# Performance work log

Measured on AMD Instinct MI355X. Metric: run time of the kernel, lower is better.

## Reference

```python
import jax, jax.numpy as jnp
import numpy as np

P = 8.0  # Lp exponent of the distance neuron (finite-p stage of l_inf-dist training)


def _patches(t, k, stride, pad):
    # [B, Cin, H, W] -> [B, Cin*k*k, H', W'], feature dim ordered channel-major
    return jax.lax.conv_general_dilated_patches(
        t, (k, k), (stride, stride), [(pad, pad), (pad, pad)])


def _lp(d):
    # d: [B, Cout, Cin*k*k, H', W'] nonnegative -> Lp norm over patch dim
    return jnp.power(jnp.sum(jnp.power(d, P), axis=2), 1.0 / P)


def norm_dist_conv(x, l, u, w, stride, pad):
    # Lp-distance "convolution": y[b,o,i,j] = || patch(x)[b,:,i,j] - w[o,:] ||_p
    # mean_normalize=True: zero-center each output unit's weight vector
    Cout, Cin, k, _ = w.shape
    wf = w.reshape(Cout, -1)
    wf = wf - jnp.mean(wf, axis=1, keepdims=True)
    wb = wf[None, :, :, None, None]                      # [1, Cout, Ckk, 1, 1]
    px = _patches(x, k, stride, pad)[:, None]            # [B, 1, Ckk, H', W']
    pl = _patches(l, k, stride, pad)[:, None]
    pu = _patches(u, k, stride, pad)[:, None]
    y = _lp(jnp.abs(px - wb))
    # interval bounds of |x_j - w_j| given x_j in [l_j, u_j], then monotone Lp
    dl = jnp.maximum(jnp.maximum(pl - wb, wb - pu), 0.0)
    du = jnp.maximum(jnp.abs(pl - wb), jnp.abs(pu - wb))
    return y, _lp(dl), _lp(du)


def bound_relu(x, l, u):
    # ReLU is monotone: apply elementwise to value and both bounds
    return jax.nn.relu(x), jax.nn.relu(l), jax.nn.relu(u)


def setup_inputs() -> dict:
    key = jax.random.key(0)
    k1, k2, k3 = jax.random.split(key, 3)
    B, C, H, W = 4, 32, 32, 32
    eps = 0.1  # l_inf perturbation radius
    x = jax.random.normal(k1, (B, C, H, W), dtype=jnp.float32)
    lower = x - eps
    upper = x + eps
    scale = 1.0 / np.sqrt(C * 9)
    weight1 = jax.random.normal(k2, (C, C, 3, 3), dtype=jnp.float32) * scale
    weight2 = jax.random.normal(k3, (C, C, 3, 3), dtype=jnp.float32) * scale
    return {"x": x, "lower": lower, "upper": upper,
            "weight1": weight1, "weight2": weight2}


def reference(x, lower, upper, weight1, weight2):
    # conv1 (stride=1, pad=1) -> BoundReLU -> conv2 -> residual add -> BoundReLU
    o = norm_dist_conv(x, lower, upper, weight1, 1, 1)
    o = bound_relu(*o)
    o = norm_dist_conv(*o, weight2, 1, 1)
    out = (o[0] + x, o[1] + lower, o[2] + upper)  # identity shortcut (stride=1, in==out)
    out = bound_relu(*out)
    return jnp.stack(out)  # [3, B, C, H, W]: (value, lower, upper)
```

## Files before the change

kernel.cpp:

```cpp
#include <hip/hip_runtime.h>
#include <hip/hip_bf16.h>

#define NB 4
#define NC 32
#define NH 32
#define NW 32
#define KK 288
#define PLANE (NB*NC*NH*NW)

__global__ __launch_bounds__(256) void prep_weights_k(
        const float* __restrict__ w1,
        const float* __restrict__ w2,
        float* __restrict__ wf1, float* __restrict__ wf2)
{
    const int row = blockIdx.x;
    const float* src = (row < NC) ? w1 : w2;
    float* dst = (row < NC) ? wf1 : wf2;
    const int co = row & (NC - 1);
    const int tid = threadIdx.x;
    __shared__ float red[256];
    const float a = (tid < KK)       ? src[co*KK + tid]       : 0.0f;
    const float b = (tid + 256 < KK) ? src[co*KK + tid + 256] : 0.0f;
    red[tid] = a + b;
    __syncthreads();
    for (int s = 128; s > 0; s >>= 1) {
        if (tid < s) red[tid] += red[tid + s];
        __syncthreads();
    }
    const float mean = red[0] * (1.0f / (float)KK);
    if (tid < KK)       dst[co*KK + tid]       = a - mean;
    if (tid + 256 < KK) dst[co*KK + tid + 256] = b - mean;
}

template<bool STAGE2>
__global__ __launch_bounds__(256) void normdist_conv_k(
    const float* __restrict__ xb,
    const float* __restrict__ lb,
    const float* __restrict__ ub,
    const float* __restrict__ my,
    const float* __restrict__ ml,
    const float* __restrict__ mu,
    const float* __restrict__ wf,
    float* __restrict__ oy, float* __restrict__ ol, float* __restrict__ ou,
    float* __restrict__ out)
{
    const int h   = blockIdx.x;
    const int cog = blockIdx.y;
    const int b   = blockIdx.z;
    const int tx  = threadIdx.x;
    const int ty  = threadIdx.y;
    const int tid = ty * 32 + tx;

    __shared__ float sX[NC*3*34];
    __shared__ float sL[NC*3*34];
    __shared__ float sU[NC*3*34];
    __shared__ float sW[8*KK];

    for (int i = tid; i < 8*KK; i += 256) sW[i] = wf[cog*8*KK + i];

    for (int i = tid; i < NC*3*34; i += 256) {
        const int c   = i / 102;
        const int rem = i - c*102;
        const int r   = rem / 34;
        const int col = rem - r*34;
        const int gh  = h + r - 1;
        const int gw  = col - 1;
        float vx = 0.0f, vl = 0.0f, vu = 0.0f;
        if ((unsigned)gh < NH && (unsigned)gw < NW) {
            const int g = ((b*NC + c)*NH + gh)*NW + gw;
            if (STAGE2) { vx = my[g]; vl = ml[g]; vu = mu[g]; }
            else        { vx = xb[g]; vl = lb[g]; vu = ub[g]; }
        }
        sX[i] = vx; sL[i] = vl; sU[i] = vu;
    }
    __syncthreads();

    float accY = 0.0f, accL = 0.0f, accU = 0.0f;
    const float* wrow = &sW[ty*KK];
    #pragma unroll 2
    for (int c = 0; c < NC; ++c) {
        #pragma unroll
        for (int r = 0; r < 3; ++r) {
            const int pb = (c*3 + r)*34 + tx;
            const int wb = c*9 + r*3;
            #pragma unroll
            for (int kw = 0; kw < 3; ++kw) {
                const float wv = wrow[wb + kw];
                const float px = sX[pb + kw];
                const float pl = sL[pb + kw];
                const float pu = sU[pb + kw];
                const float d  = px - wv;
                const float d2 = d*d, d4 = d2*d2;
                accY = fmaf(d4, d4, accY);
                const float a  = pl - wv;
                const float nb = wv - pu;
                const float m  = fmaxf(fmaxf(a, nb), 0.0f);
                const float m2 = m*m, m4 = m2*m2;
                accL = fmaf(m4, m4, accL);
                const float a2 = a*a, q2 = nb*nb;
                const float mm2 = fmaxf(a2, q2);
                const float mm4 = mm2*mm2;
                accU = fmaf(mm4, mm4, accU);
            }
        }
    }

    const float y  = sqrtf(sqrtf(sqrtf(accY)));
    const float dl = sqrtf(sqrtf(sqrtf(accL)));
    const float du = sqrtf(sqrtf(sqrtf(accU)));

    const int co = cog*8 + ty;
    const int o  = ((b*NC + co)*NH + h)*NW + tx;
    if (!STAGE2) {
        oy[o] = y; ol[o] = dl; ou[o] = du;
    } else {
        out[o]           = fmaxf(y  + xb[o], 0.0f);
        out[PLANE + o]   = fmaxf(dl + lb[o], 0.0f);
        out[2*PLANE + o] = fmaxf(du + ub[o], 0.0f);
    }
}

extern "C" void kernel_launch(void* const* d_in, const int* in_sizes, int n_in,
                              void* d_out, int out_size, void* d_ws, size_t ws_size,
                              hipStream_t stream)
{
    const float* x  = (const float*)d_in[0];
    const float* l  = (const float*)d_in[1];
    const float* u  = (const float*)d_in[2];
    const float* w1 = (const float*)d_in[3];
    const float* w2 = (const float*)d_in[4];
    float* ws  = (float*)d_ws;
    float* wf1 = ws;
    float* wf2 = ws + NC*KK;
    float* my  = ws + 2*NC*KK;
    float* ml  = my + PLANE;
    float* mu  = ml + PLANE;
    float* out = (float*)d_out;

    prep_weights_k<<<64, 256, 0, stream>>>(w1, w2, wf1, wf2);

    dim3 blk(32, 8);
    dim3 grd(NH, 4, NB);
    normdist_conv_k<false><<<grd, blk, 0, stream>>>(x, l, u, nullptr, nullptr, nullptr,
                                                    wf1, my, ml, mu, nullptr);
    normdist_conv_k<true ><<<grd, blk, 0, stream>>>(x, l, u, my, ml, mu,
                                                    wf2, nullptr, nullptr, nullptr, out);
}
```

Before: 109.9 us.

## Fuse weight mean-centering into conv kernels and pack x/l/u into float4 LDS

Removes the separate weight-preparation kernel launch: each conv block now loads raw weights and zero-centers them in shared memory with a warp-shuffle reduction. The x/lower/upper tiles are interleaved into one float4 shared array, and weights are padded to float4 per row, so the inner loop issues wide LDS loads instead of three scalar loads per tap. This trades one fewer launch and fewer LDS instructions for redundant mean computation in every block and a larger shared-memory footprint.

```diff
diff --git a/kernel.cpp b/kernel.cpp
--- a/kernel.cpp
+++ b/kernel.cpp
@@ -8,30 +8,6 @@
 #define KK 288
 #define PLANE (NB*NC*NH*NW)
 
-__global__ __launch_bounds__(256) void prep_weights_k(
-        const float* __restrict__ w1,
-        const float* __restrict__ w2,
-        float* __restrict__ wf1, float* __restrict__ wf2)
-{
-    const int row = blockIdx.x;
-    const float* src = (row < NC) ? w1 : w2;
-    float* dst = (row < NC) ? wf1 : wf2;
-    const int co = row & (NC - 1);
-    const int tid = threadIdx.x;
-    __shared__ float red[256];
-    const float a = (tid < KK)       ? src[co*KK + tid]       : 0.0f;
-    const float b = (tid + 256 < KK) ? src[co*KK + tid + 256] : 0.0f;
-    red[tid] = a + b;
-    __syncthreads();
-    for (int s = 128; s > 0; s >>= 1) {
-        if (tid < s) red[tid] += red[tid + s];
-        __syncthreads();
-    }
-    const float mean = red[0] * (1.0f / (float)KK);
-    if (tid < KK)       dst[co*KK + tid]       = a - mean;
-    if (tid + 256 < KK) dst[co*KK + tid + 256] = b - mean;
-}
-
 template<bool STAGE2>
 __global__ __launch_bounds__(256) void normdist_conv_k(
     const float* __restrict__ xb,
@@ -40,7 +16,7 @@
     const float* __restrict__ my,
     const float* __restrict__ ml,
     const float* __restrict__ mu,
-    const float* __restrict__ wf,
+    const float* __restrict__ wraw,
     float* __restrict__ oy, float* __restrict__ ol, float* __restrict__ ou,
     float* __restrict__ out)
 {
@@ -51,12 +27,19 @@
     const int ty  = threadIdx.y;
     const int tid = ty * 32 + tx;
 
-    __shared__ float sX[NC*3*34];
-    __shared__ float sL[NC*3*34];
-    __shared__ float sU[NC*3*34];
-    __shared__ float sW[8*KK];
+    __shared__ float4 sP[NC*3*34];
+    __shared__ float  sWf[8*NC*3*4];
+    float4* sW4 = (float4*)sWf;
 
-    for (int i = tid; i < 8*KK; i += 256) sW[i] = wf[cog*8*KK + i];
+    for (int i = tid; i < 8*KK; i += 256) {
+        const int co  = i / KK;
+        const int rem = i - co*KK;
+        const int c   = rem / 9;
+        const int r9  = rem - c*9;
+        const int r   = r9 / 3;
+        const int kw  = r9 - r*3;
+        sWf[((co*NC + c)*3 + r)*4 + kw] = wraw[(cog*8 + co)*KK + rem];
+    }
 
     for (int i = tid; i < NC*3*34; i += 256) {
         const int c   = i / 102;
@@ -71,38 +54,58 @@
             if (STAGE2) { vx = my[g]; vl = ml[g]; vu = mu[g]; }
             else        { vx = xb[g]; vl = lb[g]; vu = ub[g]; }
         }
-        sX[i] = vx; sL[i] = vl; sU[i] = vu;
+        sP[i] = make_float4(vx, vl, vu, 0.0f);
+    }
+    __syncthreads();
+
+    {
+        const int co = tid >> 5;
+        const int c  = tid & 31;
+        float4 a0 = sW4[(co*NC + c)*3 + 0];
+        float4 a1 = sW4[(co*NC + c)*3 + 1];
+        float4 a2 = sW4[(co*NC + c)*3 + 2];
+        float s = a0.x+a0.y+a0.z + a1.x+a1.y+a1.z + a2.x+a2.y+a2.z;
+        #pragma unroll
+        for (int off = 16; off > 0; off >>= 1) s += __shfl_xor(s, off, 32);
+        const float mean = s * (1.0f / (float)KK);
+        a0.x -= mean; a0.y -= mean; a0.z -= mean; a0.w = 0.0f;
+        a1.x -= mean; a1.y -= mean; a1.z -= mean; a1.w = 0.0f;
+        a2.x -= mean; a2.y -= mean; a2.z -= mean; a2.w = 0.0f;
+        sW4[(co*NC + c)*3 + 0] = a0;
+        sW4[(co*NC + c)*3 + 1] = a1;
+        sW4[(co*NC + c)*3 + 2] = a2;
     }
     __syncthreads();
 
     float accY = 0.0f, accL = 0.0f, accU = 0.0f;
-    const float* wrow = &sW[ty*KK];
-    #pragma unroll 2
+
+    auto tap = [&](float wv, float4 p) {
+        const float d  = p.x - wv;
+        const float d2 = d*d, d4 = d2*d2;
+        accY = fmaf(d4, d4, accY);
+        const float a  = p.y - wv;
+        const float nb = wv - p.z;
+        const float m  = fmaxf(fmaxf(a, nb), 0.0f);
+        const float m2 = m*m, m4 = m2*m2;
+        accL = fmaf(m4, m4, accL);
+        const float a2 = a*a, q2 = nb*nb;
+        const float mm2 = fmaxf(a2, q2);
+        const float mm4 = mm2*mm2;
+        accU = fmaf(mm4, mm4, accU);
+    };
+
+    #pragma unroll 4
     for (int c = 0; c < NC; ++c) {
-        #pragma unroll
-        for (int r = 0; r < 3; ++r) {
-            const int pb = (c*3 + r)*34 + tx;
-            const int wb = c*9 + r*3;
-            #pragma unroll
-            for (int kw = 0; kw < 3; ++kw) {
-                const float wv = wrow[wb + kw];
-                const float px = sX[pb + kw];
-                const float pl = sL[pb + kw];
-                const float pu = sU[pb + kw];
-                const float d  = px - wv;
-                const float d2 = d*d, d4 = d2*d2;
-                accY = fmaf(d4, d4, accY);
-                const float a  = pl - wv;
-                const float nb = wv - pu;
-                const float m  = fmaxf(fmaxf(a, nb), 0.0f);
-                const float m2 = m*m, m4 = m2*m2;
-                accL = fmaf(m4, m4, accL);
-                const float a2 = a*a, q2 = nb*nb;
-                const float mm2 = fmaxf(a2, q2);
-                const float mm4 = mm2*mm2;
-                accU = fmaf(mm4, mm4, accU);
-            }
-        }
+        const float4 w0 = sW4[(ty*NC + c)*3 + 0];
+        const float4 w1 = sW4[(ty*NC + c)*3 + 1];
+        const float4 w2 = sW4[(ty*NC + c)*3 + 2];
+        const int pb = c*3*34 + tx;
+        const float4 p00 = sP[pb +   0], p01 = sP[pb +   1], p02 = sP[pb +   2];
+        const float4 p10 = sP[pb +  34], p11 = sP[pb +  35], p12 = sP[pb +  36];
+        const float4 p20 = sP[pb +  68], p21 = sP[pb +  69], p22 = sP[pb +  70];
+        tap(w0.x, p00); tap(w0.y, p01); tap(w0.z, p02);
+        tap(w1.x, p10); tap(w1.y, p11); tap(w1.z, p12);
+        tap(w2.x, p20); tap(w2.y, p21); tap(w2.z, p22);
     }
 
     const float y  = sqrtf(sqrtf(sqrtf(accY)));
@@ -129,20 +132,16 @@
     const float* u  = (const float*)d_in[2];
     const float* w1 = (const float*)d_in[3];
     const float* w2 = (const float*)d_in[4];
-    float* ws  = (float*)d_ws;
-    float* wf1 = ws;
-    float* wf2 = ws + NC*KK;
-    float* my  = ws + 2*NC*KK;
-    float* ml  = my + PLANE;
-    float* mu  = ml + PLANE;
+    float* ws = (float*)d_ws;
+    float* my = ws;
+    float* ml = my + PLANE;
+    float* mu = ml + PLANE;
     float* out = (float*)d_out;
-
-    prep_weights_k<<<64, 256, 0, stream>>>(w1, w2, wf1, wf2);
 
     dim3 blk(32, 8);
     dim3 grd(NH, 4, NB);
     normdist_conv_k<false><<<grd, blk, 0, stream>>>(x, l, u, nullptr, nullptr, nullptr,
-                                                    wf1, my, ml, mu, nullptr);
+                                                    w1, my, ml, mu, nullptr);
     normdist_conv_k<true ><<<grd, blk, 0, stream>>>(x, l, u, my, ml, mu,
-                                                    wf2, nullptr, nullptr, nullptr, out);
+                                                    w2, nullptr, nullptr, nullptr, out);
 }
```

After: 113.3 us. 1.03x slower.

## Split input channels across blocks, interleave patches as float4, read weights from global

Applied to the files above, without the earlier changes.

Each conv kernel now splits the 32 input channels into two halves across separate blocks, doubling grid size, and writes partial Lp sums that are combined later. Stage 2 combines stage-1 partials and takes the root while loading its tile, and a new epilogue kernel combines stage-2 partials and applies residual add and ReLU. Shared memory stores x/l/u interleaved as float4, and padded weights are read as float4 from global instead of staged in LDS. This is meant to raise occupancy and parallelism, at the cost of extra partial-sum traffic and one more launch. Stage 2 also recomputes the roots redundantly for halo elements.

```diff
diff --git a/kernel.cpp b/kernel.cpp
--- a/kernel.cpp
+++ b/kernel.cpp
@@ -1,5 +1,4 @@
 #include <hip/hip_runtime.h>
-#include <hip/hip_bf16.h>
 
 #define NB 4
 #define NC 32
@@ -7,10 +6,12 @@
 #define NW 32
 #define KK 288
 #define PLANE (NB*NC*NH*NW)
+#define CHALF 16
+
+__device__ __forceinline__ float s3(float v) { return sqrtf(sqrtf(sqrtf(v))); }
 
 __global__ __launch_bounds__(256) void prep_weights_k(
-        const float* __restrict__ w1,
-        const float* __restrict__ w2,
+        const float* __restrict__ w1, const float* __restrict__ w2,
         float* __restrict__ wf1, float* __restrict__ wf2)
 {
     const int row = blockIdx.x;
@@ -19,7 +20,7 @@
     const int co = row & (NC - 1);
     const int tid = threadIdx.x;
     __shared__ float red[256];
-    const float a = (tid < KK)       ? src[co*KK + tid]       : 0.0f;
+    const float a = src[co*KK + tid];
     const float b = (tid + 256 < KK) ? src[co*KK + tid + 256] : 0.0f;
     red[tid] = a + b;
     __syncthreads();
@@ -28,37 +29,36 @@
         __syncthreads();
     }
     const float mean = red[0] * (1.0f / (float)KK);
-    if (tid < KK)       dst[co*KK + tid]       = a - mean;
-    if (tid + 256 < KK) dst[co*KK + tid + 256] = b - mean;
+    {
+        const int e = tid, c = e / 9, r9 = e - c*9, r = r9 / 3, kw = r9 - r*3;
+        dst[co*384 + ((c*3 + r) << 2) + kw] = a - mean;
+    }
+    if (tid + 256 < KK) {
+        const int e = tid + 256, c = e / 9, r9 = e - c*9, r = r9 / 3, kw = r9 - r*3;
+        dst[co*384 + ((c*3 + r) << 2) + kw] = b - mean;
+    }
 }
 
 template<bool STAGE2>
-__global__ __launch_bounds__(256) void normdist_conv_k(
-    const float* __restrict__ xb,
-    const float* __restrict__ lb,
-    const float* __restrict__ ub,
-    const float* __restrict__ my,
-    const float* __restrict__ ml,
-    const float* __restrict__ mu,
+__global__ __launch_bounds__(256, 4) void normdist_conv_k(
+    const float* __restrict__ sy,
+    const float* __restrict__ sl,
+    const float* __restrict__ su,
     const float* __restrict__ wf,
-    float* __restrict__ oy, float* __restrict__ ol, float* __restrict__ ou,
-    float* __restrict__ out)
+    float* __restrict__ pY, float* __restrict__ pL, float* __restrict__ pU)
 {
-    const int h   = blockIdx.x;
-    const int cog = blockIdx.y;
-    const int b   = blockIdx.z;
-    const int tx  = threadIdx.x;
-    const int ty  = threadIdx.y;
-    const int tid = ty * 32 + tx;
+    const int h     = blockIdx.x;
+    const int cog   = blockIdx.y >> 1;
+    const int chalf = blockIdx.y & 1;
+    const int ch0   = chalf * CHALF;
+    const int b     = blockIdx.z;
+    const int tx    = threadIdx.x;
+    const int ty    = threadIdx.y;
+    const int tid   = ty * 32 + tx;
 
-    __shared__ float sX[NC*3*34];
-    __shared__ float sL[NC*3*34];
-    __shared__ float sU[NC*3*34];
-    __shared__ float sW[8*KK];
+    __shared__ float4 sP[CHALF*3*34];
 
-    for (int i = tid; i < 8*KK; i += 256) sW[i] = wf[cog*8*KK + i];
-
-    for (int i = tid; i < NC*3*34; i += 256) {
+    for (int i = tid; i < CHALF*3*34; i += 256) {
         const int c   = i / 102;
         const int rem = i - c*102;
         const int r   = rem / 34;
@@ -67,57 +67,68 @@
         const int gw  = col - 1;
         float vx = 0.0f, vl = 0.0f, vu = 0.0f;
         if ((unsigned)gh < NH && (unsigned)gw < NW) {
-            const int g = ((b*NC + c)*NH + gh)*NW + gw;
-            if (STAGE2) { vx = my[g]; vl = ml[g]; vu = mu[g]; }
-            else        { vx = xb[g]; vl = lb[g]; vu = ub[g]; }
+            const int g = ((b*NC + ch0 + c)*NH + gh)*NW + gw;
+            if (STAGE2) {
+                vx = s3(sy[g] + sy[PLANE + g]);
+                vl = s3(sl[g] + sl[PLANE + g]);
+                vu = s3(su[g] + su[PLANE + g]);
+            } else {
+                vx = sy[g]; vl = sl[g]; vu = su[g];
+            }
         }
-        sX[i] = vx; sL[i] = vl; sU[i] = vu;
+        sP[i] = make_float4(vx, vl, vu, 0.0f);
     }
     __syncthreads();
 
+    const int co = cog*8 + ty;
+    const float4* wbase = (const float4*)wf + (co*NC + ch0)*3;
+
     float accY = 0.0f, accL = 0.0f, accU = 0.0f;
-    const float* wrow = &sW[ty*KK];
+
+    auto tap = [&](float wv, float4 p) {
+        const float d  = p.x - wv;
+        const float d2 = d*d, d4 = d2*d2;
+        accY = fmaf(d4, d4, accY);
+        const float a  = p.y - wv;
+        const float nb = wv - p.z;
+        const float m  = fmaxf(fmaxf(a, nb), 0.0f);
+        const float m2 = m*m, m4 = m2*m2;
+        accL = fmaf(m4, m4, accL);
+        const float a2 = a*a, q2 = nb*nb;
+        const float mm2 = fmaxf(a2, q2);
+        const float mm4 = mm2*mm2;
+        accU = fmaf(mm4, mm4, accU);
+    };
+
     #pragma unroll 2
-    for (int c = 0; c < NC; ++c) {
-        #pragma unroll
-        for (int r = 0; r < 3; ++r) {
-            const int pb = (c*3 + r)*34 + tx;
-            const int wb = c*9 + r*3;
-            #pragma unroll
-            for (int kw = 0; kw < 3; ++kw) {
-                const float wv = wrow[wb + kw];
-                const float px = sX[pb + kw];
-                const float pl = sL[pb + kw];
-                const float pu = sU[pb + kw];
-                const float d  = px - wv;
-                const float d2 = d*d, d4 = d2*d2;
-                accY = fmaf(d4, d4, accY);
-                const float a  = pl - wv;
-                const float nb = wv - pu;
-                const float m  = fmaxf(fmaxf(a, nb), 0.0f);
-                const float m2 = m*m, m4 = m2*m2;
-                accL = fmaf(m4, m4, accL);
-                const float a2 = a*a, q2 = nb*nb;
-                const float mm2 = fmaxf(a2, q2);
-                const float mm4 = mm2*mm2;
-                accU = fmaf(mm4, mm4, accU);
-            }
-        }
+    for (int c = 0; c < CHALF; ++c) {
+        const float4 w0 = wbase[c*3 + 0];
+        const float4 w1 = wbase[c*3 + 1];
+        const float4 w2 = wbase[c*3 + 2];
+        const int pb = c*102 + tx;
+        tap(w0.x, sP[pb +  0]); tap(w0.y, sP[pb +  1]); tap(w0.z, sP[pb +  2]);
+        tap(w1.x, sP[pb + 34]); tap(w1.y, sP[pb + 35]); tap(w1.z, sP[pb + 36]);
+        tap(w2.x, sP[pb + 68]); tap(w2.y, sP[pb + 69]); tap(w2.z, sP[pb + 70]);
     }
 
-    const float y  = sqrtf(sqrtf(sqrtf(accY)));
-    const float dl = sqrtf(sqrtf(sqrtf(accL)));
-    const float du = sqrtf(sqrtf(sqrtf(accU)));
+    const int o = ((b*NC + co)*NH + h)*NW + tx;
+    pY[chalf*PLANE + o] = accY;
+    pL[chalf*PLANE + o] = accL;
+    pU[chalf*PLANE + o] = accU;
+}
 
-    const int co = cog*8 + ty;
-    const int o  = ((b*NC + co)*NH + h)*NW + tx;
-    if (!STAGE2) {
-        oy[o] = y; ol[o] = dl; ou[o] = du;
-    } else {
-        out[o]           = fmaxf(y  + xb[o], 0.0f);
-        out[PLANE + o]   = fmaxf(dl + lb[o], 0.0f);
-        out[2*PLANE + o] = fmaxf(du + ub[o], 0.0f);
-    }
+__global__ __launch_bounds__(256) void epilogue_k(
+    const float* __restrict__ pY, const float* __restrict__ pL, const float* __restrict__ pU,
+    const float* __restrict__ x,  const float* __restrict__ l,  const float* __restrict__ u,
+    float* __restrict__ out)
+{
+    const int o = blockIdx.x*256 + threadIdx.x;
+    const float y  = s3(pY[o] + pY[PLANE + o]);
+    const float dl = s3(pL[o] + pL[PLANE + o]);
+    const float du = s3(pU[o] + pU[PLANE + o]);
+    out[o]           = fmaxf(y  + x[o], 0.0f);
+    out[PLANE + o]   = fmaxf(dl + l[o], 0.0f);
+    out[2*PLANE + o] = fmaxf(du + u[o], 0.0f);
 }
 
 extern "C" void kernel_launch(void* const* d_in, const int* in_sizes, int n_in,
@@ -131,18 +142,20 @@
     const float* w2 = (const float*)d_in[4];
     float* ws  = (float*)d_ws;
     float* wf1 = ws;
-    float* wf2 = ws + NC*KK;
-    float* my  = ws + 2*NC*KK;
-    float* ml  = my + PLANE;
-    float* mu  = ml + PLANE;
+    float* wf2 = wf1 + 12288;
+    float* p1Y = wf2 + 12288;
+    float* p1L = p1Y + 2*PLANE;
+    float* p1U = p1L + 2*PLANE;
+    float* p2Y = p1U + 2*PLANE;
+    float* p2L = p2Y + 2*PLANE;
+    float* p2U = p2L + 2*PLANE;
     float* out = (float*)d_out;
 
     prep_weights_k<<<64, 256, 0, stream>>>(w1, w2, wf1, wf2);
 
     dim3 blk(32, 8);
-    dim3 grd(NH, 4, NB);
-    normdist_conv_k<false><<<grd, blk, 0, stream>>>(x, l, u, nullptr, nullptr, nullptr,
-                                                    wf1, my, ml, mu, nullptr);
-    normdist_conv_k<true ><<<grd, blk, 0, stream>>>(x, l, u, my, ml, mu,
-                                                    wf2, nullptr, nullptr, nullptr, out);
+    dim3 grd(NH, 8, NB);
+    normdist_conv_k<false><<<grd, blk, 0, stream>>>(x, l, u, wf1, p1Y, p1L, p1U);
+    normdist_conv_k<true ><<<grd, blk, 0, stream>>>(p1Y, p1L, p1U, wf2, p2Y, p2L, p2U);
+    epilogue_k<<<PLANE/256, 256, 0, stream>>>(p2Y, p2L, p2U, x, l, u, out);
 }
```

New measurement: 107.6 us. 1.02x faster.
